# Performance work log

Measured on AMD Instinct MI355X. Metric: run time of the kernel, lower is better.

The kernel has to match this reference:

```python
import jax, jax.numpy as jnp
import numpy as np

N, E, D = 50000, 600000, 128
LN_EPS = 1e-5


def setup_inputs() -> dict:
    key = jax.random.key(0)
    ks = jax.random.split(key, 7)
    s = 1.0 / np.sqrt(D)
    x = jax.random.normal(ks[0], (N, D), dtype=jnp.float32)
    edge_index = jax.random.randint(ks[1], (2, E), 0, N, dtype=jnp.int32)
    Wq = jax.random.normal(ks[2], (D, D), dtype=jnp.float32) * s
    Wk = jax.random.normal(ks[3], (D, D), dtype=jnp.float32) * s
    Wv = jax.random.normal(ks[4], (D, D), dtype=jnp.float32) * s
    Wo = jax.random.normal(ks[5], (D, D), dtype=jnp.float32) * s
    bo = jnp.zeros((D,), dtype=jnp.float32)
    gamma = jnp.ones((D,), dtype=jnp.float32)
    beta = jnp.zeros((D,), dtype=jnp.float32)
    return {"x": x, "edge_index": edge_index, "Wq": Wq, "Wk": Wk,
            "Wv": Wv, "Wo": Wo, "bo": bo, "gamma": gamma, "beta": beta}


def reference(x, edge_index, Wq, Wk, Wv, Wo, bo, gamma, beta):
    src, dst = edge_index[0], edge_index[1]
    # gather endpoint features, project (torch Linear: y = x @ W.T)
    q = x[dst] @ Wq.T                      # [E, D]
    k = x[src] @ Wk.T                      # [E, D]
    v = x[src] @ Wv.T                      # [E, D]
    logits = jnp.sum(q * k, axis=-1, keepdims=True) / np.sqrt(D)  # [E, 1]
    msg = jax.nn.sigmoid(logits) * v       # [E, D]
    agg = jax.ops.segment_sum(msg, dst, num_segments=N)  # scatter-add -> [N, D]
    out = agg @ Wo.T + bo
    h = x + out
    # LayerNorm over last dim
    mu = jnp.mean(h, axis=-1, keepdims=True)
    var = jnp.mean(jnp.square(h - mu), axis=-1, keepdims=True)
    return (h - mu) * jax.lax.rsqrt(var + LN_EPS) * gamma + beta
```

## Files before the change

### kernel.cpp

```cpp
#include <hip/hip_runtime.h>
#include <math.h>


#define BM 64

typedef __attribute__((ext_vector_type(8))) short bfrag;
typedef __attribute__((ext_vector_type(4))) float f32x4;

__device__ __forceinline__ short f2bf(float f) {
    union { float f; unsigned u; } v; v.f = f;
    unsigned r = v.u + 0x7FFFu + ((v.u >> 16) & 1u);
    return (short)(r >> 16);
}
__device__ __forceinline__ float bf2f(short h) {
    union { unsigned u; float f; } v;
    v.u = ((unsigned)(unsigned short)h) << 16;
    return v.f;
}
__device__ __forceinline__ float2 bfpair(unsigned w) {
    union { unsigned u; float f; } lo, hi;
    lo.u = w << 16;
    hi.u = w & 0xffff0000u;
    return make_float2(lo.f, hi.f);
}

__global__ __launch_bounds__(256) void prep_weights(
    const float* __restrict__ Wq, const float* __restrict__ Wk,
    const float* __restrict__ Wv, const float* __restrict__ Wo,
    short* __restrict__ whi, short* __restrict__ wlo)
{
    int g = blockIdx.x * 256 + threadIdx.x;
    const float* Ws[4] = {Wq, Wk, Wv, Wo};
    float f = Ws[g >> 14][g & 16383];
    short h = f2bf(f);
    short l = f2bf(f - bf2f(h));
    whi[g] = h; wlo[g] = l;
}

__global__ __launch_bounds__(256) void qkv_mfma(
    const float* __restrict__ x,
    const short* __restrict__ whi, const short* __restrict__ wlo,
    float* __restrict__ Q, unsigned short* __restrict__ K16,
    unsigned short* __restrict__ V16, int N)
{
    __shared__ short xs_hi[64][136];
    __shared__ short xs_lo[64][136];

    const int tid = threadIdx.x;
    const int row0 = blockIdx.x * BM;

    #pragma unroll
    for (int i = 0; i < 8; ++i) {
        int idx = tid + 256 * i;
        int r = idx >> 5;
        int c4 = idx & 31;
        int gr = row0 + r;
        float4 val = make_float4(0.f, 0.f, 0.f, 0.f);
        if (gr < N) val = ((const float4*)(x + (size_t)gr * 128))[c4];
        short4 h, l;
        h.x = f2bf(val.x); l.x = f2bf(val.x - bf2f(h.x));
        h.y = f2bf(val.y); l.y = f2bf(val.y - bf2f(h.y));
        h.z = f2bf(val.z); l.z = f2bf(val.z - bf2f(h.z));
        h.w = f2bf(val.w); l.w = f2bf(val.w - bf2f(h.w));
        *((short4*)&xs_hi[r][c4 * 4]) = h;
        *((short4*)&xs_lo[r][c4 * 4]) = l;
    }
    __syncthreads();

    const int wid  = tid >> 6;
    const int lane = tid & 63;
    const int n16  = lane & 15;
    const int quad = lane >> 4;

    #pragma unroll 1
    for (int mat = 0; mat < 3; ++mat) {
        const short* __restrict__ WH = whi + mat * 16384;
        const short* __restrict__ WL = wlo + mat * 16384;
        const f32x4 zero = {0.f, 0.f, 0.f, 0.f};
        f32x4 acc[4][2];
        #pragma unroll
        for (int t = 0; t < 4; ++t) { acc[t][0] = zero; acc[t][1] = zero; }

        #pragma unroll
        for (int kc = 0; kc < 4; ++kc) {
            int k0 = kc * 32 + quad * 8;
            bfrag ah[4], al[4], bh[2], bl[2];
            #pragma unroll
            for (int t = 0; t < 4; ++t) {
                ah[t] = *((const bfrag*)&xs_hi[t * 16 + n16][k0]);
                al[t] = *((const bfrag*)&xs_lo[t * 16 + n16][k0]);
            }
            #pragma unroll
            for (int c = 0; c < 2; ++c) {
                int wr = (wid * 2 + c) * 16 + n16;
                bh[c] = *((const bfrag*)(WH + wr * 128 + k0));
                bl[c] = *((const bfrag*)(WL + wr * 128 + k0));
            }
            #pragma unroll
            for (int t = 0; t < 4; ++t)
                #pragma unroll
                for (int c = 0; c < 2; ++c) {
                    acc[t][c] = __builtin_amdgcn_mfma_f32_16x16x32_bf16(ah[t], bh[c], acc[t][c], 0, 0, 0);
                    acc[t][c] = __builtin_amdgcn_mfma_f32_16x16x32_bf16(al[t], bh[c], acc[t][c], 0, 0, 0);
                    acc[t][c] = __builtin_amdgcn_mfma_f32_16x16x32_bf16(ah[t], bl[c], acc[t][c], 0, 0, 0);
                }
        }
        #pragma unroll
        for (int t = 0; t < 4; ++t)
            #pragma unroll
            for (int r = 0; r < 4; ++r) {
                int grow = row0 + t * 16 + quad * 4 + r;
                if (grow < N) {
                    int c0 = (wid * 2 + 0) * 16 + n16;
                    int c1 = (wid * 2 + 1) * 16 + n16;
                    if (mat == 0) {
                        Q[(size_t)grow * 128 + c0] = acc[t][0][r];
                        Q[(size_t)grow * 128 + c1] = acc[t][1][r];
                    } else {
                        unsigned short* Cb = (mat == 1) ? K16 : V16;
                        Cb[(size_t)grow * 128 + c0] = (unsigned short)f2bf(acc[t][0][r]);
                        Cb[(size_t)grow * 128 + c1] = (unsigned short)f2bf(acc[t][1][r]);
                    }
                }
            }
    }
}

__global__ __launch_bounds__(256) void hist_kernel(
    const int* __restrict__ ei, int* __restrict__ hist, int E)
{
    int e = blockIdx.x * blockDim.x + threadIdx.x;
    if (e < E) atomicAdd(&hist[ei[E + e]], 1);
}

#define SCAN_TPB 256
#define SCAN_EPT 4

__global__ __launch_bounds__(SCAN_TPB) void scan_partial(
    const int* __restrict__ hist, int* __restrict__ offs,
    int* __restrict__ blockSums, int N)
{
    __shared__ int sdata[SCAN_TPB];
    int b = blockIdx.x;
    int t = threadIdx.x;
    int base = b * SCAN_TPB * SCAN_EPT + t * SCAN_EPT;
    int v[SCAN_EPT];
    int tot = 0;
    #pragma unroll
    for (int j = 0; j < SCAN_EPT; ++j) {
        int idx = base + j;
        v[j] = (idx < N) ? hist[idx] : 0;
        tot += v[j];
    }
    sdata[t] = tot;
    __syncthreads();
    for (int off = 1; off < SCAN_TPB; off <<= 1) {
        int xv = (t >= off) ? sdata[t - off] : 0;
        __syncthreads();
        sdata[t] += xv;
        __syncthreads();
    }
    int run = sdata[t] - tot;
    #pragma unroll
    for (int j = 0; j < SCAN_EPT; ++j) {
        int idx = base + j;
        if (idx < N) offs[idx] = run;
        run += v[j];
    }
    if (t == SCAN_TPB - 1) blockSums[b] = sdata[t];
}

__global__ __launch_bounds__(256) void scan_blocksums(int* __restrict__ blockSums, int nb)
{
    __shared__ int sdata[256];
    int t = threadIdx.x;
    int orig = (t < nb) ? blockSums[t] : 0;
    sdata[t] = orig;
    __syncthreads();
    for (int off = 1; off < 256; off <<= 1) {
        int xv = (t >= off) ? sdata[t - off] : 0;
        __syncthreads();
        sdata[t] += xv;
        __syncthreads();
    }
    if (t < nb) blockSums[t] = sdata[t] - orig;
}

__global__ __launch_bounds__(256) void scan_add(
    int* __restrict__ offs, const int* __restrict__ blockSums, int N)
{
    int idx = blockIdx.x * blockDim.x + threadIdx.x;
    if (idx < N) offs[idx] += blockSums[idx >> 10];
}

__global__ __launch_bounds__(256) void scatter_kernel(
    const int* __restrict__ ei, int* __restrict__ offs,
    int* __restrict__ ssrc, int E)
{
    int e = blockIdx.x * blockDim.x + threadIdx.x;
    if (e < E) {
        int d = ei[E + e];
        int pos = atomicAdd(&offs[d], 1);
        ssrc[pos] = ei[e];
    }
}

#define NB 8
__global__ __launch_bounds__(256) void node_agg(
    const int* __restrict__ ssrc,
    const int* __restrict__ endoffs,
    const int* __restrict__ deg,
    const float* __restrict__ Q, const unsigned short* __restrict__ K16,
    const unsigned short* __restrict__ V16,
    float* __restrict__ agg, int N)
{
    int node = blockIdx.x * 4 + (threadIdx.x >> 6);
    int lane = threadIdx.x & 63;
    if (node >= N) return;
    int end = endoffs[node];
    int start = end - deg[node];
    float2 q = *((const float2*)(Q + (size_t)node * 128 + lane * 2));
    float a0 = 0.f, a1 = 0.f;
    int i = start;
    for (; i + NB <= end; i += NB) {
        int s[NB];
        #pragma unroll
        for (int j = 0; j < NB; ++j) s[j] = ssrc[i + j];
        unsigned kw[NB], vw[NB];
        #pragma unroll
        for (int j = 0; j < NB; ++j) {
            kw[j] = *((const unsigned*)(K16 + (size_t)s[j] * 128 + lane * 2));
            vw[j] = *((const unsigned*)(V16 + (size_t)s[j] * 128 + lane * 2));
        }
        float p[NB];
        #pragma unroll
        for (int j = 0; j < NB; ++j) {
            float2 k = bfpair(kw[j]);
            p[j] = q.x * k.x + q.y * k.y;
        }
        #pragma unroll
        for (int off = 32; off > 0; off >>= 1) {
            #pragma unroll
            for (int j = 0; j < NB; ++j) p[j] += __shfl_xor(p[j], off);
        }
        #pragma unroll
        for (int j = 0; j < NB; ++j) {
            float c = 1.f / (1.f + __expf(-p[j] * 0.0883883476483184f));
            float2 v = bfpair(vw[j]);
            a0 += c * v.x; a1 += c * v.y;
        }
    }
    for (; i < end; ++i) {
        int s = ssrc[i];
        float2 k = bfpair(*((const unsigned*)(K16 + (size_t)s * 128 + lane * 2)));
        float2 v = bfpair(*((const unsigned*)(V16 + (size_t)s * 128 + lane * 2)));
        float p = q.x * k.x + q.y * k.y;
        #pragma unroll
        for (int off = 32; off > 0; off >>= 1) p += __shfl_xor(p, off);
        float c = 1.f / (1.f + __expf(-p * 0.0883883476483184f));
        a0 += c * v.x; a1 += c * v.y;
    }
    *((float2*)(agg + (size_t)node * 128 + lane * 2)) = make_float2(a0, a1);
}

__global__ __launch_bounds__(256) void out_ln_mfma(
    const float* __restrict__ agg,
    const short* __restrict__ whi, const short* __restrict__ wlo,
    const float* __restrict__ bo, const float* __restrict__ x,
    const float* __restrict__ gamma, const float* __restrict__ beta,
    float* __restrict__ out, int N)
{
    __shared__ __align__(16) char smem[64 * 136 * 2 * 2];
    short (*xs_hi)[136] = (short(*)[136])smem;
    short (*xs_lo)[136] = (short(*)[136])(smem + 64 * 136 * 2);
    float (*hs)[132]    = (float(*)[132])smem;

    const int tid = threadIdx.x;
    const int row0 = blockIdx.x * BM;

    #pragma unroll
    for (int i = 0; i < 8; ++i) {
        int idx = tid + 256 * i;
        int r = idx >> 5;
        int c4 = idx & 31;
        int gr = row0 + r;
        float4 val = make_float4(0.f, 0.f, 0.f, 0.f);
        if (gr < N) val = ((const float4*)(agg + (size_t)gr * 128))[c4];
        short4 h, l;
        h.x = f2bf(val.x); l.x = f2bf(val.x - bf2f(h.x));
        h.y = f2bf(val.y); l.y = f2bf(val.y - bf2f(h.y));
        h.z = f2bf(val.z); l.z = f2bf(val.z - bf2f(h.z));
        h.w = f2bf(val.w); l.w = f2bf(val.w - bf2f(h.w));
        *((short4*)&xs_hi[r][c4 * 4]) = h;
        *((short4*)&xs_lo[r][c4 * 4]) = l;
    }
    __syncthreads();

    const int wid  = tid >> 6;
    const int lane = tid & 63;
    const int n16  = lane & 15;
    const int quad = lane >> 4;
    const short* __restrict__ WH = whi + 3 * 16384;
    const short* __restrict__ WL = wlo + 3 * 16384;

    const f32x4 zero = {0.f, 0.f, 0.f, 0.f};
    f32x4 acc[4][2];
    #pragma unroll
    for (int t = 0; t < 4; ++t) { acc[t][0] = zero; acc[t][1] = zero; }

    #pragma unroll
    for (int kc = 0; kc < 4; ++kc) {
        int k0 = kc * 32 + quad * 8;
        bfrag ah[4], al[4], bh[2], bl[2];
        #pragma unroll
        for (int t = 0; t < 4; ++t) {
            ah[t] = *((const bfrag*)&xs_hi[t * 16 + n16][k0]);
            al[t] = *((const bfrag*)&xs_lo[t * 16 + n16][k0]);
        }
        #pragma unroll
        for (int c = 0; c < 2; ++c) {
            int wr = (wid * 2 + c) * 16 + n16;
            bh[c] = *((const bfrag*)(WH + wr * 128 + k0));
            bl[c] = *((const bfrag*)(WL + wr * 128 + k0));
        }
        #pragma unroll
        for (int t = 0; t < 4; ++t)
            #pragma unroll
            for (int c = 0; c < 2; ++c) {
                acc[t][c] = __builtin_amdgcn_mfma_f32_16x16x32_bf16(ah[t], bh[c], acc[t][c], 0, 0, 0);
                acc[t][c] = __builtin_amdgcn_mfma_f32_16x16x32_bf16(al[t], bh[c], acc[t][c], 0, 0, 0);
                acc[t][c] = __builtin_amdgcn_mfma_f32_16x16x32_bf16(ah[t], bl[c], acc[t][c], 0, 0, 0);
            }
    }
    __syncthreads();

    #pragma unroll
    for (int t = 0; t < 4; ++t)
        #pragma unroll
        for (int r = 0; r < 4; ++r) {
            hs[t * 16 + quad * 4 + r][(wid * 2 + 0) * 16 + n16] = acc[t][0][r];
            hs[t * 16 + quad * 4 + r][(wid * 2 + 1) * 16 + n16] = acc[t][1][r];
        }
    __syncthreads();

    {
        int r = tid >> 2;
        int qd = tid & 3;
        int gr = row0 + r;
        float sum = 0.f, sq = 0.f;
        #pragma unroll
        for (int c = 0; c < 32; c += 4) {
            float4 g4 = *((float4*)&hs[r][qd * 32 + c]);
            float4 b4 = *((const float4*)(bo + qd * 32 + c));
            float4 x4 = make_float4(0.f, 0.f, 0.f, 0.f);
            if (gr < N) x4 = *((const float4*)(x + (size_t)gr * 128 + qd * 32 + c));
            float4 h = make_float4(g4.x + b4.x + x4.x, g4.y + b4.y + x4.y,
                                   g4.z + b4.z + x4.z, g4.w + b4.w + x4.w);
            *((float4*)&hs[r][qd * 32 + c]) = h;
            sum += h.x + h.y + h.z + h.w;
            sq += h.x * h.x + h.y * h.y + h.z * h.z + h.w * h.w;
        }
        sum += __shfl_xor(sum, 1); sum += __shfl_xor(sum, 2);
        sq  += __shfl_xor(sq, 1);  sq  += __shfl_xor(sq, 2);
        float mu = sum * (1.f / 128.f);
        float var = sq * (1.f / 128.f) - mu * mu;
        float rs = rsqrtf(var + 1e-5f);
        if (gr < N) {
            #pragma unroll
            for (int c = 0; c < 32; c += 4) {
                float4 h = *((float4*)&hs[r][qd * 32 + c]);
                float4 g = *((const float4*)(gamma + qd * 32 + c));
                float4 b = *((const float4*)(beta + qd * 32 + c));
                float4 o = make_float4((h.x - mu) * rs * g.x + b.x,
                                       (h.y - mu) * rs * g.y + b.y,
                                       (h.z - mu) * rs * g.z + b.z,
                                       (h.w - mu) * rs * g.w + b.w);
                *((float4*)(out + (size_t)gr * 128 + qd * 32 + c)) = o;
            }
        }
    }
}

extern "C" void kernel_launch(void* const* d_in, const int* in_sizes, int n_in,
                              void* d_out, int out_size, void* d_ws, size_t ws_size,
                              hipStream_t stream) {
    const float* x     = (const float*)d_in[0];
    const int*   ei    = (const int*)d_in[1];
    const float* Wq    = (const float*)d_in[2];
    const float* Wk    = (const float*)d_in[3];
    const float* Wv    = (const float*)d_in[4];
    const float* Wo    = (const float*)d_in[5];
    const float* bo    = (const float*)d_in[6];
    const float* gamma = (const float*)d_in[7];
    const float* beta  = (const float*)d_in[8];
    const int N = in_sizes[0] / 128;
    const int E = in_sizes[1] / 2;
    const size_t ND = (size_t)N * 128;

    float* ws  = (float*)d_ws;
    float* Q   = ws;
    unsigned short* K16 = (unsigned short*)(Q + ND);
    unsigned short* V16 = K16 + ND;
    float* agg = (float*)(V16 + ND);
    int* hist      = (int*)(agg + ND);
    int* offs      = hist + N;
    int* blockSums = offs + N;
    int* ssrc      = blockSums + 256;
    short* whi     = (short*)(ssrc + E);
    short* wlo     = whi + 4 * 16384;

    hipMemsetAsync(hist, 0, (size_t)N * sizeof(int), stream);

    prep_weights<<<256, 256, 0, stream>>>(Wq, Wk, Wv, Wo, whi, wlo);

    const int gq = (N + BM - 1) / BM;
    qkv_mfma<<<gq, 256, 0, stream>>>(x, whi, wlo, Q, K16, V16, N);

    hist_kernel<<<(E + 255) / 256, 256, 0, stream>>>(ei, hist, E);
    const int nScanBlocks = (N + SCAN_TPB * SCAN_EPT - 1) / (SCAN_TPB * SCAN_EPT);
    scan_partial<<<nScanBlocks, SCAN_TPB, 0, stream>>>(hist, offs, blockSums, N);
    scan_blocksums<<<1, 256, 0, stream>>>(blockSums, nScanBlocks);
    scan_add<<<(N + 255) / 256, 256, 0, stream>>>(offs, blockSums, N);
    scatter_kernel<<<(E + 255) / 256, 256, 0, stream>>>(ei, offs, ssrc, E);

    node_agg<<<(N + 3) / 4, 256, 0, stream>>>(ssrc, offs, hist, Q, K16, V16, agg, N);

    out_ln_mfma<<<gq, 256, 0, stream>>>(agg, whi, wlo, bo, x, gamma, beta,
                                        (float*)d_out, N);
}
```

Before: 305.7 us.

## Interleave K/V storage, merge scan kernels, fuse zeroing, and mask node_agg tail

K and V are now stored interleaved in one bf16 buffer, so node_agg fetches both with a single 8-byte gather per source row instead of two 4-byte gathers. The histogram memset is folded into the weight-prep kernel, and the three-kernel scan is replaced by one single-block scan that also writes the start offsets. In node_agg the remainder loop is replaced by clamped indices with a zeroed coefficient, and most warp reductions use ds_swizzle instead of shuffles. The risks are that the single-block scan runs serially per thread over roughly 200 entries, and the masked tail loads redundant rows for low-degree nodes.

```diff
diff --git a/kernel.cpp b/kernel.cpp
--- a/kernel.cpp
+++ b/kernel.cpp
@@ -3,6 +3,7 @@
 
 
 #define BM 64
+#define NB 8
 
 typedef __attribute__((ext_vector_type(8))) short bfrag;
 typedef __attribute__((ext_vector_type(4))) float f32x4;
@@ -24,24 +25,27 @@
     return make_float2(lo.f, hi.f);
 }
 
-__global__ __launch_bounds__(256) void prep_weights(
+__global__ __launch_bounds__(256) void zero_prep(
     const float* __restrict__ Wq, const float* __restrict__ Wk,
     const float* __restrict__ Wv, const float* __restrict__ Wo,
-    short* __restrict__ whi, short* __restrict__ wlo)
+    short* __restrict__ whi, short* __restrict__ wlo,
+    int* __restrict__ hist, int NPAD)
 {
     int g = blockIdx.x * 256 + threadIdx.x;
-    const float* Ws[4] = {Wq, Wk, Wv, Wo};
-    float f = Ws[g >> 14][g & 16383];
-    short h = f2bf(f);
-    short l = f2bf(f - bf2f(h));
-    whi[g] = h; wlo[g] = l;
+    if (g < NPAD) hist[g] = 0;
+    if (g < 65536) {
+        const float* Ws[4] = {Wq, Wk, Wv, Wo};
+        float f = Ws[g >> 14][g & 16383];
+        short h = f2bf(f);
+        short l = f2bf(f - bf2f(h));
+        whi[g] = h; wlo[g] = l;
+    }
 }
 
 __global__ __launch_bounds__(256) void qkv_mfma(
     const float* __restrict__ x,
     const short* __restrict__ whi, const short* __restrict__ wlo,
-    float* __restrict__ Q, unsigned short* __restrict__ K16,
-    unsigned short* __restrict__ V16, int N)
+    float* __restrict__ Q, unsigned short* __restrict__ KV16, int N)
 {
     __shared__ short xs_hi[64][136];
     __shared__ short xs_lo[64][136];
@@ -117,9 +121,9 @@
                         Q[(size_t)grow * 128 + c0] = acc[t][0][r];
                         Q[(size_t)grow * 128 + c1] = acc[t][1][r];
                     } else {
-                        unsigned short* Cb = (mat == 1) ? K16 : V16;
-                        Cb[(size_t)grow * 128 + c0] = (unsigned short)f2bf(acc[t][0][r]);
-                        Cb[(size_t)grow * 128 + c1] = (unsigned short)f2bf(acc[t][1][r]);
+                        size_t base = (size_t)grow * 256 + (mat - 1);
+                        KV16[base + 2 * c0] = (unsigned short)f2bf(acc[t][0][r]);
+                        KV16[base + 2 * c1] = (unsigned short)f2bf(acc[t][1][r]);
                     }
                 }
             }
@@ -133,64 +137,34 @@
     if (e < E) atomicAdd(&hist[ei[E + e]], 1);
 }
 
-#define SCAN_TPB 256
-#define SCAN_EPT 4
-
-__global__ __launch_bounds__(SCAN_TPB) void scan_partial(
+__global__ __launch_bounds__(256) void scan_all(
     const int* __restrict__ hist, int* __restrict__ offs,
-    int* __restrict__ blockSums, int N)
-{
-    __shared__ int sdata[SCAN_TPB];
-    int b = blockIdx.x;
-    int t = threadIdx.x;
-    int base = b * SCAN_TPB * SCAN_EPT + t * SCAN_EPT;
-    int v[SCAN_EPT];
-    int tot = 0;
-    #pragma unroll
-    for (int j = 0; j < SCAN_EPT; ++j) {
-        int idx = base + j;
-        v[j] = (idx < N) ? hist[idx] : 0;
-        tot += v[j];
-    }
-    sdata[t] = tot;
-    __syncthreads();
-    for (int off = 1; off < SCAN_TPB; off <<= 1) {
-        int xv = (t >= off) ? sdata[t - off] : 0;
-        __syncthreads();
-        sdata[t] += xv;
-        __syncthreads();
-    }
-    int run = sdata[t] - tot;
-    #pragma unroll
-    for (int j = 0; j < SCAN_EPT; ++j) {
-        int idx = base + j;
-        if (idx < N) offs[idx] = run;
-        run += v[j];
-    }
-    if (t == SCAN_TPB - 1) blockSums[b] = sdata[t];
-}
-
-__global__ __launch_bounds__(256) void scan_blocksums(int* __restrict__ blockSums, int nb)
-{
-    __shared__ int sdata[256];
-    int t = threadIdx.x;
-    int orig = (t < nb) ? blockSums[t] : 0;
-    sdata[t] = orig;
+    int* __restrict__ starts, int NPAD)
+{
+    __shared__ int tsum[256];
+    const int t = threadIdx.x;
+    const int C = NPAD >> 8;
+    const int c0 = t * C;
+    int local = 0;
+    for (int j = 0; j < C; j += 4) {
+        int4 v = *((const int4*)(hist + c0 + j));
+        local += v.x + v.y + v.z + v.w;
+    }
+    tsum[t] = local;
     __syncthreads();
     for (int off = 1; off < 256; off <<= 1) {
-        int xv = (t >= off) ? sdata[t - off] : 0;
+        int xv = (t >= off) ? tsum[t - off] : 0;
         __syncthreads();
-        sdata[t] += xv;
+        tsum[t] += xv;
         __syncthreads();
     }
-    if (t < nb) blockSums[t] = sdata[t] - orig;
-}
-
-__global__ __launch_bounds__(256) void scan_add(
-    int* __restrict__ offs, const int* __restrict__ blockSums, int N)
-{
-    int idx = blockIdx.x * blockDim.x + threadIdx.x;
-    if (idx < N) offs[idx] += blockSums[idx >> 10];
+    int run = tsum[t] - local;
+    for (int j = 0; j < C; ++j) {
+        int idx = c0 + j;
+        offs[idx] = run;
+        starts[idx] = run;
+        run += hist[idx];
+    }
 }
 
 __global__ __launch_bounds__(256) void scatter_kernel(
@@ -205,60 +179,67 @@
     }
 }
 
-#define NB 8
 __global__ __launch_bounds__(256) void node_agg(
     const int* __restrict__ ssrc,
+    const int* __restrict__ starts,
     const int* __restrict__ endoffs,
-    const int* __restrict__ deg,
-    const float* __restrict__ Q, const unsigned short* __restrict__ K16,
-    const unsigned short* __restrict__ V16,
+    const float* __restrict__ Q, const unsigned short* __restrict__ KV16,
     float* __restrict__ agg, int N)
 {
     int node = blockIdx.x * 4 + (threadIdx.x >> 6);
     int lane = threadIdx.x & 63;
     if (node >= N) return;
+    int start = starts[node];
     int end = endoffs[node];
-    int start = end - deg[node];
     float2 q = *((const float2*)(Q + (size_t)node * 128 + lane * 2));
     float a0 = 0.f, a1 = 0.f;
-    int i = start;
-    for (; i + NB <= end; i += NB) {
+
+    for (int i = start; i < end; i += NB) {
         int s[NB];
         #pragma unroll
-        for (int j = 0; j < NB; ++j) s[j] = ssrc[i + j];
-        unsigned kw[NB], vw[NB];
-        #pragma unroll
         for (int j = 0; j < NB; ++j) {
-            kw[j] = *((const unsigned*)(K16 + (size_t)s[j] * 128 + lane * 2));
-            vw[j] = *((const unsigned*)(V16 + (size_t)s[j] * 128 + lane * 2));
-        }
+            int idx = i + j;
+            idx = (idx < end) ? idx : (end - 1);
+            s[j] = ssrc[idx];
+        }
+        uint2 w[NB];
+        #pragma unroll
+        for (int j = 0; j < NB; ++j)
+            w[j] = *((const uint2*)(KV16 + (size_t)s[j] * 256 + lane * 4));
         float p[NB];
         #pragma unroll
         for (int j = 0; j < NB; ++j) {
-            float2 k = bfpair(kw[j]);
-            p[j] = q.x * k.x + q.y * k.y;
-        }
-        #pragma unroll
-        for (int off = 32; off > 0; off >>= 1) {
-            #pragma unroll
-            for (int j = 0; j < NB; ++j) p[j] += __shfl_xor(p[j], off);
-        }
+            float2 kv0 = bfpair(w[j].x);
+            float2 kv1 = bfpair(w[j].y);
+            p[j] = q.x * kv0.x + q.y * kv1.x;
+        }
+        #pragma unroll
+        for (int j = 0; j < NB; ++j)
+            p[j] += __int_as_float(__builtin_amdgcn_ds_swizzle(__float_as_int(p[j]), 0x041F));
+        #pragma unroll
+        for (int j = 0; j < NB; ++j)
+            p[j] += __int_as_float(__builtin_amdgcn_ds_swizzle(__float_as_int(p[j]), 0x081F));
+        #pragma unroll
+        for (int j = 0; j < NB; ++j)
+            p[j] += __int_as_float(__builtin_amdgcn_ds_swizzle(__float_as_int(p[j]), 0x101F));
+        #pragma unroll
+        for (int j = 0; j < NB; ++j)
+            p[j] += __int_as_float(__builtin_amdgcn_ds_swizzle(__float_as_int(p[j]), 0x201F));
+        #pragma unroll
+        for (int j = 0; j < NB; ++j)
+            p[j] += __int_as_float(__builtin_amdgcn_ds_swizzle(__float_as_int(p[j]), 0x401F));
+        #pragma unroll
+        for (int j = 0; j < NB; ++j)
+            p[j] += __shfl_xor(p[j], 32);
+
         #pragma unroll
         for (int j = 0; j < NB; ++j) {
             float c = 1.f / (1.f + __expf(-p[j] * 0.0883883476483184f));
-            float2 v = bfpair(vw[j]);
-            a0 += c * v.x; a1 += c * v.y;
-        }
-    }
-    for (; i < end; ++i) {
-        int s = ssrc[i];
-        float2 k = bfpair(*((const unsigned*)(K16 + (size_t)s * 128 + lane * 2)));
-        float2 v = bfpair(*((const unsigned*)(V16 + (size_t)s * 128 + lane * 2)));
-        float p = q.x * k.x + q.y * k.y;
-        #pragma unroll
-        for (int off = 32; off > 0; off >>= 1) p += __shfl_xor(p, off);
-        float c = 1.f / (1.f + __expf(-p * 0.0883883476483184f));
-        a0 += c * v.x; a1 += c * v.y;
+            if (i + j >= end) c = 0.f;
+            float2 kv0 = bfpair(w[j].x);
+            float2 kv1 = bfpair(w[j].y);
+            a0 += c * kv0.y; a1 += c * kv1.y;
+        }
     }
     *((float2*)(agg + (size_t)node * 128 + lane * 2)) = make_float2(a0, a1);
 }
@@ -396,34 +377,30 @@
     const int N = in_sizes[0] / 128;
     const int E = in_sizes[1] / 2;
     const size_t ND = (size_t)N * 128;
+    const int NPAD = ((N + 1023) / 1024) * 1024;
 
     float* ws  = (float*)d_ws;
     float* Q   = ws;
-    unsigned short* K16 = (unsigned short*)(Q + ND);
-    unsigned short* V16 = K16 + ND;
-    float* agg = (float*)(V16 + ND);
-    int* hist      = (int*)(agg + ND);
-    int* offs      = hist + N;
-    int* blockSums = offs + N;
-    int* ssrc      = blockSums + 256;
-    short* whi     = (short*)(ssrc + E);
-    short* wlo     = whi + 4 * 16384;
-
-    hipMemsetAsync(hist, 0, (size_t)N * sizeof(int), stream);
-
-    prep_weights<<<256, 256, 0, stream>>>(Wq, Wk, Wv, Wo, whi, wlo);
+    unsigned short* KV16 = (unsigned short*)(Q + ND);
+    float* agg = (float*)(KV16 + 2 * ND);
+    int* hist   = (int*)(agg + ND);
+    int* offs   = hist + NPAD;
+    int* starts = offs + NPAD;
+    int* ssrc   = starts + NPAD;
+    short* whi  = (short*)(ssrc + E);
+    short* wlo  = whi + 4 * 16384;
+
+    const int gzp = ((NPAD > 65536 ? NPAD : 65536) + 255) / 256;
+    zero_prep<<<gzp, 256, 0, stream>>>(Wq, Wk, Wv, Wo, whi, wlo, hist, NPAD);
+
+    hist_kernel<<<(E + 255) / 256, 256, 0, stream>>>(ei, hist, E);
+    scan_all<<<1, 256, 0, stream>>>(hist, offs, starts, NPAD);
+    scatter_kernel<<<(E + 255) / 256, 256, 0, stream>>>(ei, offs, ssrc, E);
 
     const int gq = (N + BM - 1) / BM;
-    qkv_mfma<<<gq, 256, 0, stream>>>(x, whi, wlo, Q, K16, V16, N);
-
-    hist_kernel<<<(E + 255) / 256, 256, 0, stream>>>(ei, hist, E);
-    const int nScanBlocks = (N + SCAN_TPB * SCAN_EPT - 1) / (SCAN_TPB * SCAN_EPT);
-    scan_partial<<<nScanBlocks, SCAN_TPB, 0, stream>>>(hist, offs, blockSums, N);
-    scan_blocksums<<<1, 256, 0, stream>>>(blockSums, nScanBlocks);
-    scan_add<<<(N + 255) / 256, 256, 0, stream>>>(offs, blockSums, N);
-    scatter_kernel<<<(E + 255) / 256, 256, 0, stream>>>(ei, offs, ssrc, E);
-
-    node_agg<<<(N + 3) / 4, 256, 0, stream>>>(ssrc, offs, hist, Q, K16, V16, agg, N);
+    qkv_mfma<<<gq, 256, 0, stream>>>(x, whi, wlo, Q, KV16, N);
+
+    node_agg<<<(N + 3) / 4, 256, 0, stream>>>(ssrc, starts, offs, Q, KV16, agg, N);
 
     out_ln_mfma<<<gq, 256, 0, stream>>>(agg, whi, wlo, bo, x, gamma, beta,
                                         (float*)d_out, N);
```

After: 369.3 us. 1.21x slower.
